# Kernel tuning notes

Hardware: AMD Instinct MI355X
Metric: run time of the kernel (lower is better)

The kernel has to match this reference:

```python
import jax, jax.numpy as jnp
import numpy as np

B, T, E = 4, 2048, 1024
H, D = 16, 64  # n_heads, head_size


def setup_inputs() -> dict:
    key = jax.random.key(0)
    ks = jax.random.split(key, 6)
    s = 0.02
    x = jax.random.normal(ks[0], (B, T, E), dtype=jnp.float32)
    Wq = jax.random.normal(ks[1], (H, E, D), dtype=jnp.float32) * s
    Wk = jax.random.normal(ks[2], (H, E, D), dtype=jnp.float32) * s
    Wv = jax.random.normal(ks[3], (H, E, D), dtype=jnp.float32) * s
    Wp = jax.random.normal(ks[4], (E, E), dtype=jnp.float32) * s
    bp = jnp.zeros((E,), dtype=jnp.float32)
    return {"x": x, "Wq": Wq, "Wk": Wk, "Wv": Wv, "Wp": Wp, "bp": bp}


def reference(x, Wq, Wk, Wv, Wp, bp):
    # Per-head bias-free Q/K/V projections (vectorized over heads)
    q = jnp.einsum('bte,hed->bhtd', x, Wq)
    k = jnp.einsum('bte,hed->bhtd', x, Wk)
    v = jnp.einsum('bte,hed->bhtd', x, Wv)
    scale = 1.0 / jnp.sqrt(jnp.asarray(D, dtype=x.dtype))
    scores = jnp.einsum('bhtd,bhsd->bhts', q, k) * scale  # [B,H,T,T]
    causal = jnp.tril(jnp.ones((T, T), dtype=bool))
    scores = jnp.where(causal, scores, jnp.asarray(-jnp.inf, dtype=scores.dtype))
    attn = jax.nn.softmax(scores, axis=-1)
    out = jnp.einsum('bhts,bhsd->bhtd', attn, v)  # [B,H,T,D]
    # concat heads: 'nh b t c -> b t (nh c)'
    out = out.transpose(0, 2, 1, 3).reshape(B, T, H * D)
    # output projection (dropout p=0.0 is identity)
    return out @ Wp.T + bp
```

## Files before the change

kernel.cpp:

```cpp
#include <hip/hip_runtime.h>

typedef unsigned short u16;
typedef __attribute__((ext_vector_type(8))) short bf16x8;
typedef __attribute__((ext_vector_type(4))) short bf16x4;
typedef __attribute__((ext_vector_type(4))) float f32x4;

__device__ __forceinline__ u16 f2bf(float f) {
  unsigned u = __float_as_uint(f);
  u += 0x7FFFu + ((u >> 16) & 1u);
  return (u16)(u >> 16);
}
__device__ __forceinline__ unsigned pack2(float a, float b) {
  return (unsigned)f2bf(a) | ((unsigned)f2bf(b) << 16);
}
#if __has_builtin(__builtin_amdgcn_cvt_pk_bf16_f32)
typedef __attribute__((ext_vector_type(2))) __bf16 bf16v2;
__device__ __forceinline__ unsigned cvt_pk(float a, float b) {
  bf16v2 v = __builtin_amdgcn_cvt_pk_bf16_f32(a, b);
  return __builtin_bit_cast(unsigned, v);
}
#else
__device__ __forceinline__ unsigned cvt_pk(float a, float b) { return pack2(a, b); }
#endif
__device__ __forceinline__ uint4 pack8(float4 a, float4 b) {
  uint4 r;
  r.x = cvt_pk(a.x, a.y); r.y = cvt_pk(a.z, a.w);
  r.z = cvt_pk(b.x, b.y); r.w = cvt_pk(b.z, b.w);
  return r;
}
__device__ __forceinline__ void gload16(const void* g, void* l) {
  __builtin_amdgcn_global_load_lds(
      (const __attribute__((address_space(1))) void*)g,
      (__attribute__((address_space(3))) void*)l, 16, 0, 0);
}
__device__ __forceinline__ f32x4 mfma16(bf16x4 a, bf16x4 b, f32x4 c) {
#if __has_builtin(__builtin_amdgcn_mfma_f32_16x16x16bf16_1k)
  return __builtin_amdgcn_mfma_f32_16x16x16bf16_1k(a, b, c, 0, 0, 0);
#elif __has_builtin(__builtin_amdgcn_mfma_f32_16x16x16_bf16)
  return __builtin_amdgcn_mfma_f32_16x16x16_bf16(a, b, c, 0, 0, 0);
#else
  asm volatile("v_mfma_f32_16x16x16_bf16 %0, %1, %2, %0\n\ts_nop 2"
               : "+v"(c) : "v"(a), "v"(b));
  return c;
#endif
}

__global__ __launch_bounds__(256) void prep(
    const float* __restrict__ x, u16* __restrict__ xbf,
    const float* __restrict__ Wq, const float* __restrict__ Wk,
    const float* __restrict__ Wv, u16* __restrict__ wt,
    const float* __restrict__ Wp, u16* __restrict__ wpbf) {
  const int tid = threadIdx.x;
  const int b = blockIdx.x;
  __shared__ __align__(16) u16 tile[64 * 72];
  if (b < 4096) {
    const size_t i = (size_t)b * 256 + tid;
    const float4* p = (const float4*)(x + i * 8);
    *(uint4*)(xbf + i * 8) = pack8(p[0], p[1]);
  } else if (b < 4864) {
    const int idx = b - 4096;
    const int w = idx >> 8;
    const int mat = (idx >> 4) & 15;
    const int r0 = (idx & 15) * 64;
    const float* src = (w == 0 ? Wq : (w == 1 ? Wk : Wv)) + (size_t)mat * 1024 * 64;
    u16* dst = wt + (size_t)w * 1024 * 1024 + (size_t)mat * 1024 * 64;
#pragma unroll
    for (int i = 0; i < 2; ++i) {
      const int c = tid + i * 256;
      const int r = c >> 3, off = (c & 7) * 8;
      const float* p = src + (size_t)(r0 + r) * 64 + off;
      *(uint4*)(&tile[r * 72 + off]) = pack8(*(const float4*)p, *(const float4*)(p + 4));
    }
    __syncthreads();
#pragma unroll
    for (int i = 0; i < 2; ++i) {
      const int c = tid + i * 256;
      const int d = c >> 3, roff = (c & 7) * 8;
      bf16x8 v;
#pragma unroll
      for (int j = 0; j < 8; ++j) v[j] = (short)tile[(roff + j) * 72 + d];
      *(bf16x8*)(dst + (size_t)d * 1024 + r0 + roff) = v;
    }
  } else {
    const size_t i = (size_t)(b - 4864) * 256 + tid;
    const float4* p = (const float4*)(Wp + i * 8);
    *(uint4*)(wpbf + i * 8) = pack8(p[0], p[1]);
  }
}

template <int MODE>
__global__ __launch_bounds__(256) void gemm_bt(
    const u16* __restrict__ A, const u16* __restrict__ BT,
    u16* __restrict__ o0, u16* __restrict__ o1, u16* __restrict__ o2,
    float* __restrict__ fout, const float* __restrict__ bp) {
  __shared__ __align__(16) u16 As[2][128 * 32];
  __shared__ __align__(16) u16 Bs[2][128 * 32];
  const int tid = threadIdx.x;
  const int lane = tid & 63, wv = tid >> 6;
  const int g = lane >> 4, ln = lane & 15;
  const int wm = wv >> 1, wn = wv & 1;
  const int m0 = blockIdx.x * 128, n0 = blockIdx.y * 128;

  const f32x4 fz = {0.f, 0.f, 0.f, 0.f};
  f32x4 acc[4][4];
#pragma unroll
  for (int i = 0; i < 4; ++i)
#pragma unroll
    for (int j = 0; j < 4; ++j) acc[i][j] = fz;

  for (int k0 = 0; k0 < 1024; k0 += 64) {
    __syncthreads();
#pragma unroll
    for (int hf = 0; hf < 2; ++hf)
#pragma unroll
      for (int j = 0; j < 2; ++j) {
        const int c = j * 256 + tid;
        const int r = c >> 2, off = (c & 3) * 8;
        gload16(A + (size_t)(m0 + r) * 1024 + k0 + hf * 32 + off, &As[hf][c * 8]);
        gload16(BT + (size_t)(n0 + r) * 1024 + k0 + hf * 32 + off, &Bs[hf][c * 8]);
      }
    __syncthreads();
#pragma unroll
    for (int hf = 0; hf < 2; ++hf) {
      bf16x8 af[4], bfr[4];
#pragma unroll
      for (int rt = 0; rt < 4; ++rt)
        af[rt] = *(const bf16x8*)(&As[hf][(wm * 64 + rt * 16 + ln) * 32 + g * 8]);
#pragma unroll
      for (int ct = 0; ct < 4; ++ct)
        bfr[ct] = *(const bf16x8*)(&Bs[hf][(wn * 64 + ct * 16 + ln) * 32 + g * 8]);
#pragma unroll
      for (int rt = 0; rt < 4; ++rt)
#pragma unroll
        for (int ct = 0; ct < 4; ++ct)
          acc[rt][ct] = __builtin_amdgcn_mfma_f32_16x16x32_bf16(af[rt], bfr[ct],
                                                                acc[rt][ct], 0, 0, 0);
    }
  }

  if (MODE == 0) {
    const int which = n0 >> 10;
    const int nl0 = (n0 & 1023) + wn * 64;
    const float qs = (which == 0) ? 0.1803368801f : 1.0f;
    if (which < 2) {
      u16* outp = which == 0 ? o0 : o1;
#pragma unroll
      for (int rt = 0; rt < 4; ++rt)
#pragma unroll
        for (int ct = 0; ct < 4; ++ct) {
          const int nl = nl0 + ct * 16 + ln;
          const int h = nl >> 6, d = nl & 63;
          const unsigned p01 = cvt_pk(acc[rt][ct][0] * qs, acc[rt][ct][1] * qs);
          const unsigned p23 = cvt_pk(acc[rt][ct][2] * qs, acc[rt][ct][3] * qs);
          const u16 vv[4] = {(u16)p01, (u16)(p01 >> 16), (u16)p23, (u16)(p23 >> 16)};
#pragma unroll
          for (int r = 0; r < 4; ++r) {
            const int m = m0 + wm * 64 + rt * 16 + 4 * g + r;
            const int b = m >> 11, t = m & 2047;
            outp[(((size_t)(b * 16 + h) * 2048 + t) << 6) + d] = vv[r];
          }
        }
    } else {
#pragma unroll
      for (int rt = 0; rt < 4; ++rt) {
        const int tb = m0 + wm * 64 + rt * 16 + 4 * g;
        const int b = tb >> 11, t = tb & 2047;
#pragma unroll
        for (int ct = 0; ct < 4; ++ct) {
          const int nl = nl0 + ct * 16 + ln;
          const int h = nl >> 6, d = nl & 63;
          uint2 pv;
          pv.x = cvt_pk(acc[rt][ct][0], acc[rt][ct][1]);
          pv.y = cvt_pk(acc[rt][ct][2], acc[rt][ct][3]);
          *(uint2*)(o2 + ((size_t)((b * 16 + h) * 64 + d) << 11) + t) = pv;
        }
      }
    }
  } else {
#pragma unroll
    for (int ct = 0; ct < 4; ++ct) {
      const int n = n0 + wn * 64 + ct * 16 + ln;
      const float bias = bp[n];
#pragma unroll
      for (int rt = 0; rt < 4; ++rt)
#pragma unroll
        for (int r = 0; r < 4; ++r) {
          const int m = m0 + wm * 64 + rt * 16 + 4 * g + r;
          fout[(size_t)m * 1024 + n] = acc[rt][ct][r] + bias;
        }
    }
  }
}

__global__ __launch_bounds__(256) void attn_kernel(
    const u16* __restrict__ Q, const u16* __restrict__ K,
    const u16* __restrict__ VT, u16* __restrict__ AO) {
  const int tid = threadIdx.x;
  const int wv = tid >> 6, lane = tid & 63, g = lane >> 4, ln = lane & 15;
  const int bh = blockIdx.x;
  const int qi = 15 - blockIdx.y;
  const u16* Qb = Q + (size_t)bh * (2048 * 64);
  const u16* Kb = K + (size_t)bh * (2048 * 64);
  const u16* Vb = VT + (size_t)bh * (64 * 2048);

  __shared__ __align__(16) u16 Ks[64 * 72];
  __shared__ __align__(16) u16 Vs[64 * 72];

  const int sr0 = tid >> 3, so0 = (tid & 7) * 8;
  const int sr1 = sr0 + 32;

  uint4 kpf0 = *(const uint4*)(Kb + (size_t)sr0 * 64 + so0);
  uint4 kpf1 = *(const uint4*)(Kb + (size_t)sr1 * 64 + so0);
  uint4 vpf0 = *(const uint4*)(Vb + (size_t)sr0 * 2048 + so0);
  uint4 vpf1 = *(const uint4*)(Vb + (size_t)sr1 * 2048 + so0);

  const int b = bh >> 4, h = bh & 15;
  const short ob = 0x3F80;
  const bf16x4 ones = {ob, ob, ob, ob};
  const f32x4 fz = {0.f, 0.f, 0.f, 0.f};

  const int q0 = qi * 128;
  const int nt = 2 * qi + 2;
  const int ntw = 2 * qi + 1 + (wv >> 1);

  bf16x8 qa[2][2];
#pragma unroll
  for (int rt = 0; rt < 2; ++rt) {
    const int row = q0 + wv * 32 + rt * 16 + ln;
#pragma unroll
    for (int hh = 0; hh < 2; ++hh)
      qa[rt][hh] = *(const bf16x8*)(Qb + (size_t)row * 64 + hh * 32 + g * 8);
  }

  f32x4 oacc[2][4], lacc[2];
#pragma unroll
  for (int rt = 0; rt < 2; ++rt) {
    lacc[rt] = fz;
#pragma unroll
    for (int dt = 0; dt < 4; ++dt) oacc[rt][dt] = fz;
  }

  for (int kt = 0; kt < nt; ++kt) {
    __syncthreads();
    *(uint4*)(&Ks[sr0 * 72 + so0]) = kpf0;
    *(uint4*)(&Ks[sr1 * 72 + so0]) = kpf1;
    *(uint4*)(&Vs[sr0 * 72 + so0]) = vpf0;
    *(uint4*)(&Vs[sr1 * 72 + so0]) = vpf1;
    __syncthreads();
    if (kt + 1 < nt) {
      const int sn = (kt + 1) * 64;
      kpf0 = *(const uint4*)(Kb + (size_t)(sn + sr0) * 64 + so0);
      kpf1 = *(const uint4*)(Kb + (size_t)(sn + sr1) * 64 + so0);
      vpf0 = *(const uint4*)(Vb + (size_t)sr0 * 2048 + sn + so0);
      vpf1 = *(const uint4*)(Vb + (size_t)sr1 * 2048 + sn + so0);
    }
    if (kt < ntw) {
      const int s0 = kt * 64;
      f32x4 sfT[2][4];
#pragma unroll
      for (int st = 0; st < 4; ++st) {
        const bf16x8 kb0 = *(const bf16x8*)(&Ks[(st * 16 + ln) * 72 + g * 8]);
        const bf16x8 kb1 = *(const bf16x8*)(&Ks[(st * 16 + ln) * 72 + 32 + g * 8]);
#pragma unroll
        for (int rt = 0; rt < 2; ++rt) {
          sfT[rt][st] = __builtin_amdgcn_mfma_f32_16x16x32_bf16(kb0, qa[rt][0],
                                                                fz, 0, 0, 0);
          sfT[rt][st] = __builtin_amdgcn_mfma_f32_16x16x32_bf16(kb1, qa[rt][1],
                                                                sfT[rt][st], 0, 0, 0);
        }
      }
      const bool diag = (kt == ntw - 1);
      bf16x4 pa[2][4];
#pragma unroll
      for (int rt = 0; rt < 2; ++rt) {
        const int qloc = wv * 32 + rt * 16 + ln;
#pragma unroll
        for (int st = 0; st < 4; ++st) {
          float e[4];
#pragma unroll
          for (int r = 0; r < 4; ++r) e[r] = __builtin_amdgcn_exp2f(sfT[rt][st][r]);
          if (diag) {
            const int sloc = s0 - q0 + st * 16 + 4 * g;
#pragma unroll
            for (int r = 0; r < 4; ++r)
              if (sloc + r > qloc) e[r] = 0.f;
          }
          uint2 packed = {cvt_pk(e[0], e[1]), cvt_pk(e[2], e[3])};
          pa[rt][st] = __builtin_bit_cast(bf16x4, packed);
        }
      }
#pragma unroll
      for (int st = 0; st < 4; ++st) {
#pragma unroll
        for (int dt = 0; dt < 4; ++dt) {
          const bf16x4 vb =
              *(const bf16x4*)(&Vs[(dt * 16 + ln) * 72 + st * 16 + 4 * g]);
#pragma unroll
          for (int rt = 0; rt < 2; ++rt)
            oacc[rt][dt] = mfma16(pa[rt][st], vb, oacc[rt][dt]);
        }
#pragma unroll
        for (int rt = 0; rt < 2; ++rt)
          lacc[rt] = mfma16(pa[rt][st], ones, lacc[rt]);
      }
    }
  }
#pragma unroll
  for (int rt = 0; rt < 2; ++rt) {
    float linv[4];
#pragma unroll
    for (int r = 0; r < 4; ++r) linv[r] = 1.f / lacc[rt][r];
#pragma unroll
    for (int dt = 0; dt < 4; ++dt) {
      const unsigned p01 =
          cvt_pk(oacc[rt][dt][0] * linv[0], oacc[rt][dt][1] * linv[1]);
      const unsigned p23 =
          cvt_pk(oacc[rt][dt][2] * linv[2], oacc[rt][dt][3] * linv[3]);
      const u16 vv[4] = {(u16)p01, (u16)(p01 >> 16), (u16)p23, (u16)(p23 >> 16)};
#pragma unroll
      for (int r = 0; r < 4; ++r) {
        const int qg = q0 + wv * 32 + rt * 16 + 4 * g + r;
        AO[(size_t)(b * 2048 + qg) * 1024 + h * 64 + dt * 16 + ln] = vv[r];
      }
    }
  }
}

extern "C" void kernel_launch(void* const* d_in, const int* in_sizes, int n_in,
                              void* d_out, int out_size, void* d_ws, size_t ws_size,
                              hipStream_t stream) {
  const float* x  = (const float*)d_in[0];
  const float* Wq = (const float*)d_in[1];
  const float* Wk = (const float*)d_in[2];
  const float* Wv = (const float*)d_in[3];
  const float* Wp = (const float*)d_in[4];
  const float* bp = (const float*)d_in[5];
  float* out = (float*)d_out;

  char* ws = (char*)d_ws;
  const size_t MB = 1048576;
  u16* xbf  = (u16*)(ws);
  u16* aows = (u16*)(ws);
  u16* wt   = (u16*)(ws + 16 * MB);
  u16* wpbf = (u16*)(ws + 22 * MB);
  u16* qws  = (u16*)(ws + 24 * MB);
  u16* kws  = (u16*)(ws + 40 * MB);
  u16* vtws = (u16*)(ws + 56 * MB);

  prep<<<dim3(5376), 256, 0, stream>>>(x, xbf, Wq, Wk, Wv, wt, Wp, wpbf);
  gemm_bt<0><<<dim3(64, 24), 256, 0, stream>>>(xbf, wt, qws, kws, vtws,
                                               nullptr, nullptr);
  attn_kernel<<<dim3(64, 16), 256, 0, stream>>>(qws, kws, vtws, aows);
  gemm_bt<1><<<dim3(64, 8), 256, 0, stream>>>(aows, wpbf, nullptr, nullptr,
                                              nullptr, out, bp);
}
```

Measured before the change: 265.4 us.

## Pair complementary causal query tiles in one 512-thread attention block

Each attention block now holds two 128-row query tiles, a long one (15-jb) and a short one (jb). Eight waves share the K/V tiles staged in LDS, so every K/V tile loaded serves both query tiles and the causal work per block is balanced. The grid halves to 64x8 blocks of 512 threads. The short tile's waves sit idle during later iterations but still join each barrier, and the larger blocks may lower occupancy.

```diff
diff --git a/kernel.cpp b/kernel.cpp
--- a/kernel.cpp
+++ b/kernel.cpp
@@ -192,13 +192,15 @@
   }
 }
 
-__global__ __launch_bounds__(256) void attn_kernel(
+__global__ __launch_bounds__(512) void attn_kernel(
     const u16* __restrict__ Q, const u16* __restrict__ K,
     const u16* __restrict__ VT, u16* __restrict__ AO) {
   const int tid = threadIdx.x;
   const int wv = tid >> 6, lane = tid & 63, g = lane >> 4, ln = lane & 15;
+  const int wvl = wv & 3;
   const int bh = blockIdx.x;
-  const int qi = 15 - blockIdx.y;
+  const int jb = blockIdx.y;
+  const int qi = (wv < 4) ? (15 - jb) : jb;
   const u16* Qb = Q + (size_t)bh * (2048 * 64);
   const u16* Kb = K + (size_t)bh * (2048 * 64);
   const u16* Vb = VT + (size_t)bh * (64 * 2048);
@@ -206,13 +208,11 @@
   __shared__ __align__(16) u16 Ks[64 * 72];
   __shared__ __align__(16) u16 Vs[64 * 72];
 
-  const int sr0 = tid >> 3, so0 = (tid & 7) * 8;
-  const int sr1 = sr0 + 32;
-
-  uint4 kpf0 = *(const uint4*)(Kb + (size_t)sr0 * 64 + so0);
-  uint4 kpf1 = *(const uint4*)(Kb + (size_t)sr1 * 64 + so0);
-  uint4 vpf0 = *(const uint4*)(Vb + (size_t)sr0 * 2048 + so0);
-  uint4 vpf1 = *(const uint4*)(Vb + (size_t)sr1 * 2048 + so0);
+  const int sr = tid >> 3;
+  const int so = (tid & 7) * 8;
+
+  uint4 kpf = *(const uint4*)(Kb + (size_t)sr * 64 + so);
+  uint4 vpf = *(const uint4*)(Vb + (size_t)sr * 2048 + so);
 
   const int b = bh >> 4, h = bh & 15;
   const short ob = 0x3F80;
@@ -220,13 +220,13 @@
   const f32x4 fz = {0.f, 0.f, 0.f, 0.f};
 
   const int q0 = qi * 128;
-  const int nt = 2 * qi + 2;
-  const int ntw = 2 * qi + 1 + (wv >> 1);
+  const int nt = 2 * (15 - jb) + 2;
+  const int ntw = 2 * qi + 1 + (wvl >> 1);
 
   bf16x8 qa[2][2];
 #pragma unroll
   for (int rt = 0; rt < 2; ++rt) {
-    const int row = q0 + wv * 32 + rt * 16 + ln;
+    const int row = q0 + wvl * 32 + rt * 16 + ln;
 #pragma unroll
     for (int hh = 0; hh < 2; ++hh)
       qa[rt][hh] = *(const bf16x8*)(Qb + (size_t)row * 64 + hh * 32 + g * 8);
@@ -242,17 +242,13 @@
 
   for (int kt = 0; kt < nt; ++kt) {
     __syncthreads();
-    *(uint4*)(&Ks[sr0 * 72 + so0]) = kpf0;
-    *(uint4*)(&Ks[sr1 * 72 + so0]) = kpf1;
-    *(uint4*)(&Vs[sr0 * 72 + so0]) = vpf0;
-    *(uint4*)(&Vs[sr1 * 72 + so0]) = vpf1;
+    *(uint4*)(&Ks[sr * 72 + so]) = kpf;
+    *(uint4*)(&Vs[sr * 72 + so]) = vpf;
     __syncthreads();
     if (kt + 1 < nt) {
       const int sn = (kt + 1) * 64;
-      kpf0 = *(const uint4*)(Kb + (size_t)(sn + sr0) * 64 + so0);
-      kpf1 = *(const uint4*)(Kb + (size_t)(sn + sr1) * 64 + so0);
-      vpf0 = *(const uint4*)(Vb + (size_t)sr0 * 2048 + sn + so0);
-      vpf1 = *(const uint4*)(Vb + (size_t)sr1 * 2048 + sn + so0);
+      kpf = *(const uint4*)(Kb + (size_t)(sn + sr) * 64 + so);
+      vpf = *(const uint4*)(Vb + (size_t)sr * 2048 + sn + so);
     }
     if (kt < ntw) {
       const int s0 = kt * 64;
@@ -273,7 +269,7 @@
       bf16x4 pa[2][4];
 #pragma unroll
       for (int rt = 0; rt < 2; ++rt) {
-        const int qloc = wv * 32 + rt * 16 + ln;
+        const int qloc = wvl * 32 + rt * 16 + ln;
 #pragma unroll
         for (int st = 0; st < 4; ++st) {
           float e[4];
@@ -319,7 +315,7 @@
       const u16 vv[4] = {(u16)p01, (u16)(p01 >> 16), (u16)p23, (u16)(p23 >> 16)};
 #pragma unroll
       for (int r = 0; r < 4; ++r) {
-        const int qg = q0 + wv * 32 + rt * 16 + 4 * g + r;
+        const int qg = q0 + wvl * 32 + rt * 16 + 4 * g + r;
         AO[(size_t)(b * 2048 + qg) * 1024 + h * 64 + dt * 16 + ln] = vv[r];
       }
     }
@@ -350,7 +346,7 @@
   prep<<<dim3(5376), 256, 0, stream>>>(x, xbf, Wq, Wk, Wv, wt, Wp, wpbf);
   gemm_bt<0><<<dim3(64, 24), 256, 0, stream>>>(xbf, wt, qws, kws, vtws,
                                                nullptr, nullptr);
-  attn_kernel<<<dim3(64, 16), 256, 0, stream>>>(qws, kws, vtws, aows);
+  attn_kernel<<<dim3(64, 8), 512, 0, stream>>>(qws, kws, vtws, aows);
   gemm_bt<1><<<dim3(64, 8), 256, 0, stream>>>(aows, wpbf, nullptr, nullptr,
                                               nullptr, out, bp);
 }
```

New measurement: 269.9 us. Within noise of the previous version (+1.7%).
